# Kernel tuning notes

Hardware: AMD Instinct MI355X
Metric: run time of the kernel (lower is better)

## Reference

```python
import jax, jax.numpy as jnp
import numpy as np

B, S, H = 32, 256, 128
K, C, DSUB, O = 8, 4096, 16, 6  # PQ subspaces, ncentroids=4096, subvector dim, bits/symbol


def setup_inputs() -> dict:
    key = jax.random.key(0)
    ks = jax.random.split(key, 8)
    return {
        "z": jax.random.normal(ks[0], (B, S, 3), jnp.float32),
        "W1": jax.random.normal(ks[1], (3, H), jnp.float32) * 0.3,
        "b1": jax.random.normal(ks[2], (H,), jnp.float32) * 0.1,
        "W2": jax.random.normal(ks[3], (H, H), jnp.float32) * 0.1,
        "b2": jax.random.normal(ks[4], (H,), jnp.float32) * 0.1,
        "centroids": jax.random.normal(ks[5], (K, C, DSUB), jnp.float32),
        "W3": jax.random.normal(ks[6], (H, O), jnp.float32) * 0.1,
        "b3": jax.random.normal(ks[7], (O,), jnp.float32) * 0.1,
    }


def reference(z, W1, b1, W2, b2, centroids, W3, b3):
    # Small demapper MLP (layers 1-2, exact dense math)
    h1 = jax.nn.relu(z @ W1 + b1)            # [B,S,H]
    h2 = jax.nn.relu(h1 @ W2 + b2)           # [B,S,H] == layer3in
    N = B * S
    x = h2.reshape(N, K, DSUB)               # split rows into K PQ subvectors
    # Encode: nearest centroid per subspace (||x-c||^2 argmin; ||x||^2 is constant per row)
    dots = jnp.einsum("nkd,kcd->nkc", x, centroids)      # [N,K,C]
    c_norm = jnp.sum(centroids * centroids, axis=-1)      # [K,C]
    codes = jnp.argmin(c_norm[None, :, :] - 2.0 * dots, axis=-1)  # [N,K] int
    # LUT: precomputed centroid @ W3 per subspace
    W3r = W3.reshape(K, DSUB, O)
    lut = jnp.einsum("kcd,kdo->kco", centroids, W3r)      # [K,C,O]
    # Approximate matmul: sum of LUT entries selected by codes
    approx = jnp.sum(lut[jnp.arange(K)[None, :], codes], axis=1)  # [N,O]
    llr = (approx + b3).reshape(B, S * O)                 # [B, n]
    return llr
```

## Files before the change

### kernel.cpp

```cpp
#include <hip/hip_runtime.h>
#include <hip/hip_fp16.h>
#include <stdint.h>

#define NROWS 8192
#define HDIM  128
#define KSUB  8
#define NC    4096
#define DSUB  16
#define OUTD  6

#define FB_TAU 3e-4f

typedef _Float16 f16x8 __attribute__((ext_vector_type(8)));
typedef float    f32x16 __attribute__((ext_vector_type(16)));

#define XK_OFF 0u
#define CN_OFF 4194304u
#define B2_OFF 4325376u
#define PK_OFF 6422528u

__global__ __launch_bounds__(256) void prep_kernel(
    const float* __restrict__ z, const float* __restrict__ W1, const float* __restrict__ b1,
    const float* __restrict__ W2, const float* __restrict__ b2,
    const float* __restrict__ ce,
    float* __restrict__ xk, float* __restrict__ cnorm, f16x8* __restrict__ B2S)
{
    __shared__ float h1s[32 * HDIM];
    __shared__ float w2s[HDIM * HDIM];
    const int t = threadIdx.x;
    const int row0 = blockIdx.x * 32;

    #pragma unroll
    for (int q = 0; q < 2; ++q) {
        const int e = blockIdx.x * 512 + q * 256 + t;
        const int k    = e >> 14;
        const int unit = (e >> 7) & 127;
        const int half = (e >> 6) & 1;
        const int lane = e & 63;
        const int n    = unit * 32 + (lane & 31);
        const int dims = (lane >> 5) * 8;
        const float* cp = &ce[((size_t)k * NC + n) * DSUB + dims];
        f16x8 hi, lo;
        #pragma unroll
        for (int j = 0; j < 8; ++j) {
            const float s = cp[j] * -16.0f;
            const _Float16 h = (_Float16)s;
            hi[j] = h;
            lo[j] = (_Float16)(s - (float)h);
        }
        B2S[e] = half ? lo : hi;
    }

    if (blockIdx.x < (KSUB * NC) / 256) {
        const int g = blockIdx.x * 256 + t;
        const float4* cp = (const float4*)&ce[(size_t)g * DSUB];
        float nn = 0.f;
        #pragma unroll
        for (int q = 0; q < 4; ++q) {
            const float4 v = cp[q];
            nn = fmaf(v.x, v.x, nn); nn = fmaf(v.y, v.y, nn);
            nn = fmaf(v.z, v.z, nn); nn = fmaf(v.w, v.w, nn);
        }
        cnorm[g] = nn;
    }

    {
        const float4* g4 = (const float4*)W2;
        float4* s4 = (float4*)w2s;
        #pragma unroll
        for (int q = 0; q < 16; ++q) s4[t + q * 256] = g4[t + q * 256];
    }

    #pragma unroll
    for (int e = 0; e < 16; ++e) {
        const int idx = e * 256 + t;
        const int r = idx >> 7, j = idx & 127;
        const int n = row0 + r;
        float acc = b1[j];
        acc = fmaf(z[n * 3 + 0], W1[0 * HDIM + j], acc);
        acc = fmaf(z[n * 3 + 1], W1[1 * HDIM + j], acc);
        acc = fmaf(z[n * 3 + 2], W1[2 * HDIM + j], acc);
        h1s[idx] = fmaxf(acc, 0.f);
    }
    __syncthreads();

    const int c4 = (t & 31) * 4;
    const int r4 = (t >> 5) * 4;
    float acc[4][4];
    #pragma unroll
    for (int a = 0; a < 4; ++a)
        #pragma unroll
        for (int b = 0; b < 4; ++b) acc[a][b] = 0.f;

    for (int k4 = 0; k4 < HDIM; k4 += 4) {
        float hh[4][4], ww[4][4];
        #pragma unroll
        for (int q = 0; q < 4; ++q) {
            const float4 v = *(const float4*)&h1s[(r4 + q) * HDIM + k4];
            hh[q][0] = v.x; hh[q][1] = v.y; hh[q][2] = v.z; hh[q][3] = v.w;
        }
        #pragma unroll
        for (int p = 0; p < 4; ++p) {
            const float4 v = *(const float4*)&w2s[(k4 + p) * HDIM + c4];
            ww[p][0] = v.x; ww[p][1] = v.y; ww[p][2] = v.z; ww[p][3] = v.w;
        }
        #pragma unroll
        for (int q = 0; q < 4; ++q)
            #pragma unroll
            for (int p = 0; p < 4; ++p) {
                acc[q][0] = fmaf(hh[q][p], ww[p][0], acc[q][0]);
                acc[q][1] = fmaf(hh[q][p], ww[p][1], acc[q][1]);
                acc[q][2] = fmaf(hh[q][p], ww[p][2], acc[q][2]);
                acc[q][3] = fmaf(hh[q][p], ww[p][3], acc[q][3]);
            }
    }

    const float4 bb = *(const float4*)&b2[c4];
    const int kk = c4 >> 4;
    const int dd = c4 & 15;
    #pragma unroll
    for (int q = 0; q < 4; ++q) {
        float4 o;
        o.x = fmaxf(acc[q][0] + bb.x, 0.f);
        o.y = fmaxf(acc[q][1] + bb.y, 0.f);
        o.z = fmaxf(acc[q][2] + bb.z, 0.f);
        o.w = fmaxf(acc[q][3] + bb.w, 0.f);
        *(float4*)&xk[((size_t)kk * NROWS + (row0 + r4 + q)) * DSUB + dd] = o;
    }
}

__global__ __launch_bounds__(256, 4) void argmin_kernel(
    const float* __restrict__ xk, const f16x8* __restrict__ B2S,
    const float* __restrict__ cnorm, unsigned long long* __restrict__ pk)
{
    __shared__ f16x8 cs[8 * 2 * 64];
    __shared__ float cnS[2048];
    const int t = threadIdx.x;
    const int lane = t & 63;
    const int wid  = t >> 6;
    const int k  = blockIdx.y;
    const int cz = blockIdx.z;
    const int rowbase = blockIdx.x * 128 + wid * 32;
    const int col = lane & 31;
    const int khl = lane >> 5;

    {
        const float* cnp0 = &cnorm[k * NC + cz * 2048];
        #pragma unroll
        for (int q = 0; q < 8; ++q) cnS[t + q * 256] = cnp0[t + q * 256] * 2048.0f;
    }

    f16x8 Ah, Al;
    {
        const float* xp = &xk[((size_t)k * NROWS + rowbase + col) * DSUB + khl * 8];
        #pragma unroll
        for (int j = 0; j < 8; ++j) {
            const float s = xp[j] * 256.0f;
            const _Float16 h = (_Float16)s;
            Ah[j] = h;
            Al[j] = (_Float16)(s - (float)h);
        }
    }

    float m1[16], m2[16];
    int   idx[16];
    #pragma unroll
    for (int r = 0; r < 16; ++r) { m1[r] = 1e30f; m2[r] = 1e30f; idx[r] = 0; }

    const f16x8* gB = &B2S[((size_t)(k * 128 + cz * 64)) * 128];

    for (int ch = 0; ch < 8; ++ch) {
        __syncthreads();
        {
            const uint4* g4 = (const uint4*)gB + ch * 1024;
            uint4* s4 = (uint4*)cs;
            #pragma unroll
            for (int q = 0; q < 4; ++q) s4[t + q * 256] = g4[t + q * 256];
        }
        __syncthreads();

        #pragma unroll 2
        for (int u = 0; u < 8; ++u) {
            const f16x8 Bh = cs[u * 128 + lane];
            const f16x8 Bl = cs[u * 128 + 64 + lane];
            const float nrmS = cnS[(ch * 8 + u) * 32 + col];
            f32x16 acc;
            #pragma unroll
            for (int r = 0; r < 16; ++r) acc[r] = nrmS;
            acc = __builtin_amdgcn_mfma_f32_32x32x16_f16(Ah, Bh, acc, 0, 0, 0);
            acc = __builtin_amdgcn_mfma_f32_32x32x16_f16(Al, Bl, acc, 0, 0, 0);
            acc = __builtin_amdgcn_mfma_f32_32x32x16_f16(Ah, Bl, acc, 0, 0, 0);
            acc = __builtin_amdgcn_mfma_f32_32x32x16_f16(Al, Bh, acc, 0, 0, 0);
            const int c = cz * 2048 + (ch * 8 + u) * 32 + col;
            #pragma unroll
            for (int r = 0; r < 16; ++r) {
                const float s = acc[r];
                const bool lt = s < m1[r];
                m2[r] = __builtin_amdgcn_fmed3f(s, m1[r], m2[r]);
                idx[r] = lt ? c : idx[r];
                m1[r] = fminf(s, m1[r]);
            }
        }
    }

    #pragma unroll
    for (int off = 1; off < 32; off <<= 1) {
        #pragma unroll
        for (int r = 0; r < 16; ++r) {
            const float om1 = __shfl_xor(m1[r], off, 64);
            const float om2 = __shfl_xor(m2[r], off, 64);
            const int  oidx = __shfl_xor(idx[r], off, 64);
            const bool better = (om1 < m1[r]) ||
                                (om1 == m1[r] && oidx < idx[r]);
            m2[r] = fminf(fminf(m2[r], om2), fmaxf(m1[r], om1));
            m1[r] = better ? om1 : m1[r];
            idx[r] = better ? oidx : idx[r];
        }
    }

    if (col == 0) {
        #pragma unroll
        for (int r = 0; r < 16; ++r) {
            const int row = rowbase + (r & 3) + 8 * (r >> 2) + 4 * khl;
            const float m1t = m1[r] * (1.0f / 2048.0f);
            unsigned u = __float_as_uint(m1t);
            u = (u & 0x80000000u) ? ~u : (u | 0x80000000u);
            const unsigned short dh = __half_as_ushort(
                __float2half((m2[r] - m1[r]) * (1.0f / 2048.0f)));
            pk[((size_t)cz * NROWS + row) * KSUB + k] =
                ((unsigned long long)u << 32) |
                ((unsigned)dh << 16) | (unsigned)idx[r];
        }
    }
}

__global__ __launch_bounds__(256) void finish_kernel(
    const float* __restrict__ xk, const float* __restrict__ ce,
    const float* __restrict__ cnorm, const unsigned long long* __restrict__ pk,
    const float* __restrict__ W3, const float* __restrict__ b3,
    float* __restrict__ out)
{
    __shared__ int codes_s[256];
    __shared__ int wl_s[256];
    __shared__ int wcnt;
    const int t = threadIdx.x;
    const int row0 = blockIdx.x * 32;
    if (t == 0) wcnt = 0;
    __syncthreads();

    {
        const int row = row0 + (t >> 3);
        const int k = t & 7;
        const unsigned long long a = pk[(size_t)row * KSUB + k];
        const unsigned long long b = pk[((size_t)NROWS + row) * KSUB + k];
        const unsigned long long w = a < b ? a : b;
        const unsigned long long l = a < b ? b : a;
        const unsigned uw = (unsigned)(w >> 32), ul = (unsigned)(l >> 32);
        const float m1w = __uint_as_float((uw & 0x80000000u) ? (uw ^ 0x80000000u) : ~uw);
        const float m1l = __uint_as_float((ul & 0x80000000u) ? (ul ^ 0x80000000u) : ~ul);
        const float m2g = fminf(
            m1w + (float)__ushort_as_half((unsigned short)((unsigned)w >> 16)), m1l);
        codes_s[t] = (int)(w & 0xFFFFull);
        if (m2g - m1w < FB_TAU) {
            const int slot = atomicAdd(&wcnt, 1);
            wl_s[slot] = t;
        }
    }
    __syncthreads();

    {
        const int lane = t & 63;
        const int wid = t >> 6;
        const int nitems = wcnt;
        for (int i = wid; i < nitems; i += 4) {
            const int wg = wl_s[i];
            const int row = row0 + (wg >> 3), k = wg & 7;
            float xr[DSUB];
            {
                const float* xp = &xk[((size_t)k * NROWS + row) * DSUB];
                #pragma unroll
                for (int q = 0; q < DSUB; q += 4) {
                    const float4 v = *(const float4*)&xp[q];
                    xr[q + 0] = -2.f * v.x; xr[q + 1] = -2.f * v.y;
                    xr[q + 2] = -2.f * v.z; xr[q + 3] = -2.f * v.w;
                }
            }
            float bm = 1e30f; int bi = NC;
            for (int c = lane; c < NC; c += 64) {
                const float* cp = &ce[((size_t)k * NC + c) * DSUB];
                float s = cnorm[k * NC + c];
                #pragma unroll
                for (int d = 0; d < DSUB; ++d) s = fmaf(xr[d], cp[d], s);
                if (s < bm) { bm = s; bi = c; }
            }
            #pragma unroll
            for (int off = 1; off < 64; off <<= 1) {
                const float om = __shfl_xor(bm, off, 64);
                const int  oi = __shfl_xor(bi, off, 64);
                const bool better = (om < bm) || (om == bm && oi < bi);
                bm = better ? om : bm;
                bi = better ? oi : bi;
            }
            if (lane == 0) codes_s[wg] = bi;
        }
    }
    __syncthreads();

    if (t < 32 * OUTD) {
        const int nl = t / OUTD;
        const int o = t - nl * OUTD;
        const int n = row0 + nl;
        float acc = b3[o];
        #pragma unroll
        for (int k = 0; k < KSUB; ++k) {
            const int code = codes_s[nl * KSUB + k];
            const float* cp = &ce[((size_t)k * NC + code) * DSUB];
            const float* wp = &W3[(k * DSUB) * OUTD + o];
            #pragma unroll
            for (int d = 0; d < DSUB; ++d)
                acc = fmaf(cp[d], wp[d * OUTD], acc);
        }
        out[n * OUTD + o] = acc;
    }
}

extern "C" void kernel_launch(void* const* d_in, const int* in_sizes, int n_in,
                              void* d_out, int out_size, void* d_ws, size_t ws_size,
                              hipStream_t stream)
{
    const float* z  = (const float*)d_in[0];
    const float* W1 = (const float*)d_in[1];
    const float* b1 = (const float*)d_in[2];
    const float* W2 = (const float*)d_in[3];
    const float* b2 = (const float*)d_in[4];
    const float* ce = (const float*)d_in[5];
    const float* W3 = (const float*)d_in[6];
    const float* b3 = (const float*)d_in[7];

    char* ws = (char*)d_ws;
    float* xk    = (float*)(ws + XK_OFF);
    float* cnorm = (float*)(ws + CN_OFF);
    f16x8* B2S   = (f16x8*)(ws + B2_OFF);
    unsigned long long* pk = (unsigned long long*)(ws + PK_OFF);

    hipLaunchKernelGGL(prep_kernel, dim3(256), dim3(256), 0, stream,
                       z, W1, b1, W2, b2, ce, xk, cnorm, B2S);
    hipLaunchKernelGGL(argmin_kernel, dim3(64, 8, 2), dim3(256), 0, stream,
                       xk, B2S, cnorm, pk);
    hipLaunchKernelGGL(finish_kernel, dim3(256), dim3(256), 0, stream,
                       xk, ce, cnorm, pk, W3, b3, (float*)d_out);
}
```

Baseline: 175.2 us.

## Split argmin centroids four ways and double-buffer centroid tiles in LDS

The argmin kernel now splits the 4096 centroids into four z-slices instead of two, which doubles the grid to 2048 blocks. Inside each block, centroid tiles are register-prefetched and double-buffered in shared memory, so the global loads for the next chunk overlap the MFMA and min-tracking work on the current one. The finish kernel now merges four partial packed minima per row and subspace, and recomputes the second-best gap used for the fallback test. In exchange, each block redoes the same per-block setup of A loads and norms and writes twice as many partial results, and the larger shared buffer may limit occupancy.

```diff
diff --git a/kernel.cpp b/kernel.cpp
--- a/kernel.cpp
+++ b/kernel.cpp
@@ -133,8 +133,8 @@
     const float* __restrict__ xk, const f16x8* __restrict__ B2S,
     const float* __restrict__ cnorm, unsigned long long* __restrict__ pk)
 {
-    __shared__ f16x8 cs[8 * 2 * 64];
-    __shared__ float cnS[2048];
+    __shared__ f16x8 cs[2][8 * 2 * 64];
+    __shared__ float cnS[1024];
     const int t = threadIdx.x;
     const int lane = t & 63;
     const int wid  = t >> 6;
@@ -145,9 +145,9 @@
     const int khl = lane >> 5;
 
     {
-        const float* cnp0 = &cnorm[k * NC + cz * 2048];
-        #pragma unroll
-        for (int q = 0; q < 8; ++q) cnS[t + q * 256] = cnp0[t + q * 256] * 2048.0f;
+        const float* cnp0 = &cnorm[k * NC + cz * 1024];
+        #pragma unroll
+        for (int q = 0; q < 4; ++q) cnS[t + q * 256] = cnp0[t + q * 256] * 2048.0f;
     }
 
     f16x8 Ah, Al;
@@ -167,22 +167,30 @@
     #pragma unroll
     for (int r = 0; r < 16; ++r) { m1[r] = 1e30f; m2[r] = 1e30f; idx[r] = 0; }
 
-    const f16x8* gB = &B2S[((size_t)(k * 128 + cz * 64)) * 128];
-
-    for (int ch = 0; ch < 8; ++ch) {
-        __syncthreads();
-        {
-            const uint4* g4 = (const uint4*)gB + ch * 1024;
-            uint4* s4 = (uint4*)cs;
-            #pragma unroll
-            for (int q = 0; q < 4; ++q) s4[t + q * 256] = g4[t + q * 256];
-        }
-        __syncthreads();
-
+    const uint4* gB = (const uint4*)&B2S[((size_t)(k * 128 + cz * 32)) * 128];
+
+    uint4 pf[4];
+    #pragma unroll
+    for (int q = 0; q < 4; ++q) pf[q] = gB[t + q * 256];
+    {
+        uint4* s4 = (uint4*)cs[0];
+        #pragma unroll
+        for (int q = 0; q < 4; ++q) s4[t + q * 256] = pf[q];
+    }
+    __syncthreads();
+
+    for (int ch = 0; ch < 4; ++ch) {
+        if (ch < 3) {
+            const uint4* gp = gB + (ch + 1) * 1024;
+            #pragma unroll
+            for (int q = 0; q < 4; ++q) pf[q] = gp[t + q * 256];
+        }
+
+        const f16x8* buf = cs[ch & 1];
         #pragma unroll 2
         for (int u = 0; u < 8; ++u) {
-            const f16x8 Bh = cs[u * 128 + lane];
-            const f16x8 Bl = cs[u * 128 + 64 + lane];
+            const f16x8 Bh = buf[u * 128 + lane];
+            const f16x8 Bl = buf[u * 128 + 64 + lane];
             const float nrmS = cnS[(ch * 8 + u) * 32 + col];
             f32x16 acc;
             #pragma unroll
@@ -191,7 +199,7 @@
             acc = __builtin_amdgcn_mfma_f32_32x32x16_f16(Al, Bl, acc, 0, 0, 0);
             acc = __builtin_amdgcn_mfma_f32_32x32x16_f16(Ah, Bl, acc, 0, 0, 0);
             acc = __builtin_amdgcn_mfma_f32_32x32x16_f16(Al, Bh, acc, 0, 0, 0);
-            const int c = cz * 2048 + (ch * 8 + u) * 32 + col;
+            const int c = cz * 1024 + (ch * 8 + u) * 32 + col;
             #pragma unroll
             for (int r = 0; r < 16; ++r) {
                 const float s = acc[r];
@@ -200,6 +208,14 @@
                 idx[r] = lt ? c : idx[r];
                 m1[r] = fminf(s, m1[r]);
             }
+        }
+
+        if (ch < 3) {
+            __syncthreads();
+            uint4* s4 = (uint4*)cs[(ch + 1) & 1];
+            #pragma unroll
+            for (int q = 0; q < 4; ++q) s4[t + q * 256] = pf[q];
+            __syncthreads();
         }
     }
 
@@ -251,15 +267,24 @@
     {
         const int row = row0 + (t >> 3);
         const int k = t & 7;
-        const unsigned long long a = pk[(size_t)row * KSUB + k];
-        const unsigned long long b = pk[((size_t)NROWS + row) * KSUB + k];
-        const unsigned long long w = a < b ? a : b;
-        const unsigned long long l = a < b ? b : a;
-        const unsigned uw = (unsigned)(w >> 32), ul = (unsigned)(l >> 32);
+        unsigned long long p[4];
+        #pragma unroll
+        for (int s = 0; s < 4; ++s)
+            p[s] = pk[((size_t)s * NROWS + row) * KSUB + k];
+        unsigned long long w = p[0];
+        #pragma unroll
+        for (int s = 1; s < 4; ++s) w = p[s] < w ? p[s] : w;
+        const unsigned uw = (unsigned)(w >> 32);
         const float m1w = __uint_as_float((uw & 0x80000000u) ? (uw ^ 0x80000000u) : ~uw);
-        const float m1l = __uint_as_float((ul & 0x80000000u) ? (ul ^ 0x80000000u) : ~ul);
-        const float m2g = fminf(
-            m1w + (float)__ushort_as_half((unsigned short)((unsigned)w >> 16)), m1l);
+        float m2g = m1w + (float)__ushort_as_half((unsigned short)((unsigned)w >> 16));
+        #pragma unroll
+        for (int s = 0; s < 4; ++s) {
+            if (p[s] != w) {
+                const unsigned us = (unsigned)(p[s] >> 32);
+                m2g = fminf(m2g, __uint_as_float(
+                    (us & 0x80000000u) ? (us ^ 0x80000000u) : ~us));
+            }
+        }
         codes_s[t] = (int)(w & 0xFFFFull);
         if (m2g - m1w < FB_TAU) {
             const int slot = atomicAdd(&wcnt, 1);
@@ -345,7 +370,7 @@
 
     hipLaunchKernelGGL(prep_kernel, dim3(256), dim3(256), 0, stream,
                        z, W1, b1, W2, b2, ce, xk, cnorm, B2S);
-    hipLaunchKernelGGL(argmin_kernel, dim3(64, 8, 2), dim3(256), 0, stream,
+    hipLaunchKernelGGL(argmin_kernel, dim3(64, 8, 4), dim3(256), 0, stream,
                        xk, B2S, cnorm, pk);
     hipLaunchKernelGGL(finish_kernel, dim3(256), dim3(256), 0, stream,
                        xk, ce, cnorm, pk, W3, b3, (float*)d_out);
```

Result: slower. 187.7 us (+7.1%).
